# Optimization experiments

Measured on AMD Instinct MI355X. Metric: run time of the kernel, lower is better.

The kernel has to match this reference:

```python
import jax, jax.numpy as jnp
import numpy as np

N_NODES = 100000
N_EDGES = 1600000
IN_CH = 128
OUT_CH = 128
HEADS = 4
HEAD_DIM = OUT_CH // HEADS
NEG_SLOPE_ATT = 0.2   # GATConv default negative_slope
NEG_SLOPE_ACT = 0.2   # block's LeakyReLU(0.2)
BN_EPS = 1e-5


def setup_inputs() -> dict:
    key = jax.random.key(0)
    ks = jax.random.split(key, 6)
    x = jax.random.normal(ks[0], (N_NODES, IN_CH), dtype=jnp.float32)
    edge_index = jax.random.randint(ks[1], (2, N_EDGES), 0, N_NODES, dtype=jnp.int64)
    W = jax.random.normal(ks[2], (IN_CH, HEADS * HEAD_DIM), dtype=jnp.float32) * (1.0 / np.sqrt(IN_CH))
    att_src = jax.random.normal(ks[3], (HEADS, HEAD_DIM), dtype=jnp.float32) * 0.1
    att_dst = jax.random.normal(ks[4], (HEADS, HEAD_DIM), dtype=jnp.float32) * 0.1
    bias = jnp.zeros((OUT_CH,), dtype=jnp.float32)
    gamma = jnp.ones((OUT_CH,), dtype=jnp.float32)
    beta = jnp.zeros((OUT_CH,), dtype=jnp.float32)
    return {"x": x, "edge_index": edge_index, "W": W, "att_src": att_src,
            "att_dst": att_dst, "bias": bias, "gamma": gamma, "beta": beta}


def reference(x, edge_index, W, att_src, att_dst, bias, gamma, beta):
    N = x.shape[0]
    H, C = att_src.shape
    src, dst = edge_index[0], edge_index[1]

    # linear projection per head: [N, H, C]
    h = (x @ W).reshape(N, H, C)

    # per-node attention contributions (alpha_src[i] + alpha_dst[j] on edges)
    a_src = jnp.einsum('nhc,hc->nh', h, att_src)  # [N, H]
    a_dst = jnp.einsum('nhc,hc->nh', h, att_dst)  # [N, H]

    # per-edge raw score, leaky relu (GAT attention nonlinearity)
    e = jax.nn.leaky_relu(a_src[src] + a_dst[dst], NEG_SLOPE_ATT)  # [E, H]

    # segment softmax over edges grouped by destination node
    e_max = jax.ops.segment_max(e, dst, num_segments=N)            # [N, H]
    e_max = jnp.where(jnp.isfinite(e_max), e_max, 0.0)
    ex = jnp.exp(e - e_max[dst])                                   # [E, H]
    denom = jax.ops.segment_sum(ex, dst, num_segments=N)           # [N, H]
    alpha = ex / (denom[dst] + 1e-16)                              # [E, H]

    # scatter-add aggregation of alpha-weighted source features
    msg = alpha[:, :, None] * h[src]                               # [E, H, C]
    out = jax.ops.segment_sum(msg, dst, num_segments=N)            # [N, H, C]
    out = out.reshape(N, H * C) + bias                             # concat heads + bias

    # BatchNorm1d (training mode: batch statistics, biased variance)
    mu = out.mean(axis=0)
    var = out.var(axis=0)
    out = (out - mu) * jax.lax.rsqrt(var + BN_EPS) * gamma + beta

    return jax.nn.leaky_relu(out, NEG_SLOPE_ACT)
```

## Files before the change

### kernel.cpp

```cpp
#include <hip/hip_runtime.h>
#include <hip/hip_fp16.h>
#include <math.h>


#define WAVE  64
#define SHIFT 8
#define CAP   4608
#define CPAD  16
#define FBLK  512

__device__ __forceinline__ float4 leaky4(float4 v, float s) {
    v.x = v.x > 0.f ? v.x : s * v.x;
    v.y = v.y > 0.f ? v.y : s * v.y;
    v.z = v.z > 0.f ? v.z : s * v.z;
    v.w = v.w > 0.f ? v.w : s * v.w;
    return v;
}

__global__ __launch_bounds__(256) void k_gemm_att(
    const float* __restrict__ x, const float* __restrict__ W,
    const float* __restrict__ att_src, const float* __restrict__ att_dst,
    __half* __restrict__ h16, float* __restrict__ a_src, float* __restrict__ a_dst,
    int* __restrict__ cursor, int czero, int N)
{
    __shared__ float xsT[128][36];
    __shared__ float Wl[64][128];

    const int t = threadIdx.x;
    const int row0 = blockIdx.x * 32;

    if (blockIdx.x == 0) {
        for (int i = t; i < czero; i += 256) cursor[i] = 0;
    }

    {
        const int r  = t >> 3;
        const int k0 = (t & 7) * 16;
        const int rr = min(row0 + r, N - 1);
        const float4* xp = (const float4*)(x + (size_t)rr * 128 + k0);
        float4 v0 = xp[0], v1 = xp[1], v2 = xp[2], v3 = xp[3];
        float tmp[16] = {v0.x,v0.y,v0.z,v0.w, v1.x,v1.y,v1.z,v1.w,
                         v2.x,v2.y,v2.z,v2.w, v3.x,v3.y,v3.z,v3.w};
        #pragma unroll
        for (int i = 0; i < 16; ++i) xsT[k0 + i][r] = tmp[i];
    }

    const int tx = t & 31;
    const int ty = t >> 5;
    float acc[4][4] = {{0.f}};

    for (int kt = 0; kt < 2; ++kt) {
        __syncthreads();
        {
            const float4* wp = (const float4*)(W + kt * 64 * 128);
            float4* wl = (float4*)&Wl[0][0];
            #pragma unroll
            for (int i = 0; i < 8; ++i) wl[t + 256 * i] = wp[t + 256 * i];
        }
        __syncthreads();
        #pragma unroll
        for (int k = 0; k < 64; ++k) {
            float4 wv = *(const float4*)&Wl[k][tx * 4];
            float4 xv = *(const float4*)&xsT[kt * 64 + k][ty * 4];
            float xa[4] = {xv.x, xv.y, xv.z, xv.w};
            float wa[4] = {wv.x, wv.y, wv.z, wv.w};
            #pragma unroll
            for (int i = 0; i < 4; ++i)
                #pragma unroll
                for (int j = 0; j < 4; ++j)
                    acc[i][j] = fmaf(xa[i], wa[j], acc[i][j]);
        }
    }

    const int head = tx >> 3;
    const float4 s4 = *(const float4*)&att_src[head * 32 + (tx & 7) * 4];
    const float4 d4 = *(const float4*)&att_dst[head * 32 + (tx & 7) * 4];

    #pragma unroll
    for (int i = 0; i < 4; ++i) {
        const int n = row0 + ty * 4 + i;
        if (n < N) {
            union { __half2 h2[2]; uint2 u; } pk;
            pk.h2[0] = __floats2half2_rn(acc[i][0], acc[i][1]);
            pk.h2[1] = __floats2half2_rn(acc[i][2], acc[i][3]);
            *(uint2*)(h16 + (size_t)n * 128 + tx * 4) = pk.u;
        }
        float ss = acc[i][0]*s4.x + acc[i][1]*s4.y + acc[i][2]*s4.z + acc[i][3]*s4.w;
        float dd = acc[i][0]*d4.x + acc[i][1]*d4.y + acc[i][2]*d4.z + acc[i][3]*d4.w;
        #pragma unroll
        for (int off = 1; off < 8; off <<= 1) {
            ss += __shfl_xor(ss, off);
            dd += __shfl_xor(dd, off);
        }
        if ((tx & 7) == 0 && n < N) {
            a_src[n * 4 + head] = ss;
            a_dst[n * 4 + head] = dd;
        }
    }
}

__global__ __launch_bounds__(256) void k_bucket(
    const int* __restrict__ src, const int* __restrict__ dst,
    int* __restrict__ cursor, int* __restrict__ pairs, int E, int nbkt)
{
    __shared__ int hist[512];
    __shared__ int lcur[512];
    const int t = threadIdx.x;
    hist[t] = 0; hist[t + 256] = 0;
    __syncthreads();

    const int base = blockIdx.x * 2048;
    int sr[8], dr[8];
    #pragma unroll
    for (int i = 0; i < 8; ++i) {
        const int e = base + i * 256 + t;
        if (e < E) { sr[i] = src[e]; dr[i] = dst[e]; }
        else       { sr[i] = -1;     dr[i] = -1; }
    }
    #pragma unroll
    for (int i = 0; i < 8; ++i)
        if (dr[i] >= 0) atomicAdd(&hist[dr[i] >> SHIFT], 1);
    __syncthreads();

    for (int b = t; b < nbkt; b += 256) {
        const int hcount = hist[b];
        lcur[b] = (hcount > 0) ? atomicAdd(&cursor[b * CPAD], hcount) + b * CAP
                               : b * CAP;
    }
    __syncthreads();

    #pragma unroll
    for (int i = 0; i < 8; ++i) {
        if (dr[i] >= 0) {
            const int b = dr[i] >> SHIFT;
            const int pos = atomicAdd(&lcur[b], 1);
            if (pos < b * CAP + CAP)
                pairs[pos] = sr[i] | ((dr[i] & 255) << 20);
        }
    }
}

__global__ __launch_bounds__(FBLK) void k_fine(
    const int* __restrict__ cursor, const int* __restrict__ pairs,
    int* __restrict__ offsets, int* __restrict__ deg,
    int* __restrict__ perm_src, float* __restrict__ bn_sums, int N)
{
    __shared__ int stage[CAP];
    __shared__ int cnt[256];
    __shared__ int scn[256];
    __shared__ int cur[256];

    const int t = threadIdx.x;
    const int b = blockIdx.x;

    if (b == 0 && t < 256) bn_sums[t] = 0.f;

    const int cnt_b = min(cursor[b * CPAD], CAP);
    const int pbase = b * CAP;

    if (t < 256) cnt[t] = 0;
    __syncthreads();

    for (int i = t; i < cnt_b; i += FBLK) {
        const int v = pairs[pbase + i];
        stage[i] = v;
        atomicAdd(&cnt[v >> 20], 1);
    }
    __syncthreads();

    const int v0 = (t < 256) ? cnt[t] : 0;
    if (t < 256) scn[t] = v0;
    __syncthreads();
    for (int off = 1; off < 256; off <<= 1) {
        const int add = (t < 256 && t >= off) ? scn[t - off] : 0;
        __syncthreads();
        if (t < 256) scn[t] += add;
        __syncthreads();
    }
    if (t < 256) {
        const int excl = scn[t] - v0;
        const int node = (b << SHIFT) + t;
        if (node < N) {
            offsets[node] = pbase + excl;
            deg[node]     = v0;
        }
        cur[t] = pbase + excl;
    }
    __syncthreads();

    for (int i = t; i < cnt_b; i += FBLK) {
        const int v = stage[i];
        const int pos = atomicAdd(&cur[v >> 20], 1);
        perm_src[pos] = v & 0xFFFFF;
    }
}

__global__ __launch_bounds__(256) void k_aggregate(
    const int* __restrict__ offsets, const int* __restrict__ deg,
    const int* __restrict__ perm_src,
    const float* __restrict__ a_src, const float* __restrict__ a_dst,
    const __half* __restrict__ h16, float* __restrict__ out, int N)
{
    __shared__ int    ls_s [4][2][32];
    __shared__ float4 ls_ex[4][2][32];

    const int wv   = threadIdx.x >> 6;
    const int lane = threadIdx.x & 63;
    const int nd   = lane >> 5;
    const int l32  = lane & 31;
    const int n    = blockIdx.x * 8 + wv * 2 + nd;
    const bool valid = (n < N);

    const int beg = valid ? offsets[n] : 0;
    const int dg  = valid ? deg[n]     : 0;
    const float4 ad = valid ? *(const float4*)(a_dst + n * 4)
                            : make_float4(0.f, 0.f, 0.f, 0.f);

    const int ph  = (lane >> 4) & 1;
    const int l16 = lane & 15;
    const int ch  = l16 * 8;
    const int hd  = l16 >> 2;
    float acc[8] = {0.f,0.f,0.f,0.f,0.f,0.f,0.f,0.f};
    float dsum = 0.f;

    const int dgmax = max(dg, __shfl_xor(dg, 32));

    for (int base = 0; base < dgmax; base += 32) {
        const int idx = base + l32;
        int s = 0;
        float4 ex = make_float4(0.f, 0.f, 0.f, 0.f);
        if (idx < dg) {
            s = perm_src[beg + idx];
            float4 as = *(const float4*)(a_src + s * 4);
            float4 e = leaky4(make_float4(as.x+ad.x, as.y+ad.y, as.z+ad.z, as.w+ad.w), 0.2f);
            ex.x = __expf(e.x); ex.y = __expf(e.y);
            ex.z = __expf(e.z); ex.w = __expf(e.w);
        }
        ls_s [wv][nd][l32] = s;
        ls_ex[wv][nd][l32] = ex;

        int cn = dg - base;
        cn = (cn < 0) ? 0 : ((cn > 32) ? 32 : cn);
        const int cnmax = max(cn, __shfl_xor(cn, 32));
        const int cnr = (cnmax + 3) & ~3;

        #pragma unroll 2
        for (int t = 0; t < cnr; t += 2) {
            const int slot = t + ph;
            const int   sj  = ls_s[wv][nd][slot];
            const float exj = ((const float*)&ls_ex[wv][nd][slot])[hd];
            union { uint4 u; __half2 h2[4]; } pk;
            pk.u = *(const uint4*)(h16 + (size_t)sj * 128 + ch);
            acc[0] = fmaf(__low2float (pk.h2[0]), exj, acc[0]);
            acc[1] = fmaf(__high2float(pk.h2[0]), exj, acc[1]);
            acc[2] = fmaf(__low2float (pk.h2[1]), exj, acc[2]);
            acc[3] = fmaf(__high2float(pk.h2[1]), exj, acc[3]);
            acc[4] = fmaf(__low2float (pk.h2[2]), exj, acc[4]);
            acc[5] = fmaf(__high2float(pk.h2[2]), exj, acc[5]);
            acc[6] = fmaf(__low2float (pk.h2[3]), exj, acc[6]);
            acc[7] = fmaf(__high2float(pk.h2[3]), exj, acc[7]);
            dsum += exj;
        }
    }

    #pragma unroll
    for (int c = 0; c < 8; ++c) acc[c] += __shfl_xor(acc[c], 16);
    dsum += __shfl_xor(dsum, 16);

    if (ph == 0 && valid) {
        const float inv = 1.0f / (dsum + 1e-16f);
        float* op = out + (size_t)n * 128 + ch;
        *(float4*)(op)     = make_float4(acc[0]*inv, acc[1]*inv, acc[2]*inv, acc[3]*inv);
        *(float4*)(op + 4) = make_float4(acc[4]*inv, acc[5]*inv, acc[6]*inv, acc[7]*inv);
    }
}

__global__ __launch_bounds__(256) void k_bnstats(const float* __restrict__ out,
                                                 float* __restrict__ sums, int N)
{
    const int c    = threadIdx.x & 127;
    const int half = threadIdx.x >> 7;
    float s = 0.f, sq = 0.f;
    for (int r = blockIdx.x * 2 + half; r < N; r += gridDim.x * 2) {
        float v = out[(size_t)r * 128 + c];
        s += v;
        sq = fmaf(v, v, sq);
    }
    __shared__ float ls[256], lq[256];
    ls[threadIdx.x] = s; lq[threadIdx.x] = sq;
    __syncthreads();
    if (half == 0) {
        s  += ls[threadIdx.x + 128];
        sq += lq[threadIdx.x + 128];
        atomicAdd(&sums[c], s);
        atomicAdd(&sums[128 + c], sq);
    }
}

__global__ __launch_bounds__(256) void k_bnapply(float* __restrict__ out,
                                                 const float* __restrict__ sums,
                                                 const float* __restrict__ gamma,
                                                 const float* __restrict__ beta,
                                                 int N)
{
    const int i = blockIdx.x * 256 + threadIdx.x;
    const int total = N * 128;
    if (i >= total) return;
    const int c = i & 127;
    const float invN = 1.0f / (float)N;
    float mu  = sums[c] * invN;
    float var = sums[128 + c] * invN - mu * mu;
    float v = out[i];
    float y = (v - mu) * rsqrtf(var + 1e-5f) * gamma[c] + beta[c];
    out[i] = y > 0.f ? y : 0.2f * y;
}

extern "C" void kernel_launch(void* const* d_in, const int* in_sizes, int n_in,
                              void* d_out, int out_size, void* d_ws, size_t ws_size,
                              hipStream_t stream)
{
    const float* x     = (const float*)d_in[0];
    const int*   ei    = (const int*)  d_in[1];
    const float* W     = (const float*)d_in[2];
    const float* att_s = (const float*)d_in[3];
    const float* att_d = (const float*)d_in[4];
    const float* gamma = (const float*)d_in[6];
    const float* beta  = (const float*)d_in[7];
    float* out = (float*)d_out;

    const int N = in_sizes[0] / 128;
    const int E = in_sizes[1] / 2;
    const int nbkt = (N + (1 << SHIFT) - 1) >> SHIFT;

    char* ws = (char*)d_ws;
    size_t off = 0;
    auto carve = [&](size_t bytes) {
        char* p = ws + off;
        off += (bytes + 255) & ~(size_t)255;
        return p;
    };
    __half* h16      = (__half*)carve((size_t)N * 128 * 2);
    float* a_src     = (float*)carve((size_t)N * 4 * 4);
    float* a_dst     = (float*)carve((size_t)N * 4 * 4);
    int*   offsets   = (int*)  carve((size_t)N * 4);
    int*   deg       = (int*)  carve((size_t)N * 4);
    int*   cursor    = (int*)  carve((size_t)nbkt * CPAD * 4);
    float* bn_sums   = (float*)carve(256 * 4);
    int*   pairs     = (int*)  carve((size_t)nbkt * CAP * 4);
    int*   perm_src  = (int*)  carve((size_t)nbkt * CAP * 4);

    k_gemm_att<<<(N + 31) / 32, 256, 0, stream>>>(x, W, att_s, att_d, h16, a_src, a_dst,
                                                  cursor, nbkt * CPAD, N);
    k_bucket<<<(E + 2047) / 2048, 256, 0, stream>>>(ei, ei + E, cursor, pairs, E, nbkt);
    k_fine<<<nbkt, FBLK, 0, stream>>>(cursor, pairs, offsets, deg, perm_src, bn_sums, N);
    k_aggregate<<<(N + 7) / 8, 256, 0, stream>>>(offsets, deg, perm_src, a_src, a_dst, h16, out, N);
    k_bnstats<<<512, 256, 0, stream>>>(out, bn_sums, N);
    k_bnapply<<<(N * 128 + 255) / 256, 256, 0, stream>>>(out, bn_sums, gamma, beta, N);
}
```

Before: 339.7 us.

## Use split-bf16 MFMA for projection GEMM and move attention dots to separate kernel

Replaces the FP32 FMA tiled GEMM with MFMA bf16 instructions, using a hi/lo split (three MFMAs per tile) to approximate FP32 accuracy. Each block now handles 128 rows, and W is converted to bf16 hi/lo in shared memory once per block. The per-node attention scores are now computed by a new kernel that reads back the fp16 h, rather than in the GEMM epilogue. This adds an extra launch and an extra pass over h, uses the fp16-rounded h for the attention scores, and the h16 stores become scalar 2-byte writes.

```diff
diff --git a/kernel.cpp b/kernel.cpp
--- a/kernel.cpp
+++ b/kernel.cpp
@@ -8,6 +8,9 @@
 #define CAP   4608
 #define CPAD  16
 #define FBLK  512
+
+typedef __attribute__((ext_vector_type(8))) short short8v;
+typedef __attribute__((ext_vector_type(4))) float f32x4;
 
 __device__ __forceinline__ float4 leaky4(float4 v, float s) {
     v.x = v.x > 0.f ? v.x : s * v.x;
@@ -17,85 +20,134 @@
     return v;
 }
 
-__global__ __launch_bounds__(256) void k_gemm_att(
+__device__ __forceinline__ unsigned short f2bf(float f) {
+    unsigned int u = __float_as_uint(f);
+    u += 0x7FFFu + ((u >> 16) & 1u);
+    return (unsigned short)(u >> 16);
+}
+__device__ __forceinline__ float bf2f(unsigned short h) {
+    return __uint_as_float(((unsigned int)h) << 16);
+}
+__device__ __forceinline__ void cvt8(float4 a, float4 b, short8v& hi, short8v& lo) {
+    float f[8] = {a.x, a.y, a.z, a.w, b.x, b.y, b.z, b.w};
+    #pragma unroll
+    for (int j = 0; j < 8; ++j) {
+        unsigned short h = f2bf(f[j]);
+        hi[j] = (short)h;
+        lo[j] = (short)f2bf(f[j] - bf2f(h));
+    }
+}
+
+__global__ __launch_bounds__(256) void k_gemm(
     const float* __restrict__ x, const float* __restrict__ W,
-    const float* __restrict__ att_src, const float* __restrict__ att_dst,
-    __half* __restrict__ h16, float* __restrict__ a_src, float* __restrict__ a_dst,
-    int* __restrict__ cursor, int czero, int N)
-{
-    __shared__ float xsT[128][36];
-    __shared__ float Wl[64][128];
+    __half* __restrict__ h16, int* __restrict__ cursor, int czero, int N)
+{
+    __shared__ short8v WB[2][32][64];
 
     const int t = threadIdx.x;
-    const int row0 = blockIdx.x * 32;
-
     if (blockIdx.x == 0) {
         for (int i = t; i < czero; i += 256) cursor[i] = 0;
     }
 
     {
-        const int r  = t >> 3;
-        const int k0 = (t & 7) * 16;
-        const int rr = min(row0 + r, N - 1);
-        const float4* xp = (const float4*)(x + (size_t)rr * 128 + k0);
-        float4 v0 = xp[0], v1 = xp[1], v2 = xp[2], v3 = xp[3];
-        float tmp[16] = {v0.x,v0.y,v0.z,v0.w, v1.x,v1.y,v1.z,v1.w,
-                         v2.x,v2.y,v2.z,v2.w, v3.x,v3.y,v3.z,v3.w};
+        const int lane = t & 63;
+        const int w    = t >> 6;
         #pragma unroll
-        for (int i = 0; i < 16; ++i) xsT[k0 + i][r] = tmp[i];
-    }
-
-    const int tx = t & 31;
-    const int ty = t >> 5;
-    float acc[4][4] = {{0.f}};
-
-    for (int kt = 0; kt < 2; ++kt) {
-        __syncthreads();
-        {
-            const float4* wp = (const float4*)(W + kt * 64 * 128);
-            float4* wl = (float4*)&Wl[0][0];
+        for (int rep = 0; rep < 8; ++rep) {
+            const int region = rep * 4 + w;
+            const int kt = region >> 3, n = region & 7;
+            const int krow = kt * 32 + ((lane >> 4) << 3);
+            const int col  = n * 16 + (lane & 15);
+            short8v hi, lo;
             #pragma unroll
-            for (int i = 0; i < 8; ++i) wl[t + 256 * i] = wp[t + 256 * i];
-        }
-        __syncthreads();
+            for (int j = 0; j < 8; ++j) {
+                const float wv = W[(krow + j) * 128 + col];
+                const unsigned short hb = f2bf(wv);
+                hi[j] = (short)hb;
+                lo[j] = (short)f2bf(wv - bf2f(hb));
+            }
+            WB[0][region][lane] = hi;
+            WB[1][region][lane] = lo;
+        }
+    }
+    __syncthreads();
+
+    const int lane = t & 63;
+    const int wv_  = t >> 6;
+    const int jcol = lane & 15;
+    const int rg   = lane >> 4;
+    const int rowbase = blockIdx.x * 128 + wv_ * 32;
+
+    const int arow0 = min(rowbase + jcol,      N - 1);
+    const int arow1 = min(rowbase + 16 + jcol, N - 1);
+
+    f32x4 acc0[8] = {};
+    f32x4 acc1[8] = {};
+
+    #pragma unroll
+    for (int kt = 0; kt < 4; ++kt) {
+        const int k0 = kt * 32 + rg * 8;
+        const float* xp0 = x + (size_t)arow0 * 128 + k0;
+        const float* xp1 = x + (size_t)arow1 * 128 + k0;
+        short8v ah0, al0, ah1, al1;
+        cvt8(*(const float4*)xp0, *(const float4*)(xp0 + 4), ah0, al0);
+        cvt8(*(const float4*)xp1, *(const float4*)(xp1 + 4), ah1, al1);
         #pragma unroll
-        for (int k = 0; k < 64; ++k) {
-            float4 wv = *(const float4*)&Wl[k][tx * 4];
-            float4 xv = *(const float4*)&xsT[kt * 64 + k][ty * 4];
-            float xa[4] = {xv.x, xv.y, xv.z, xv.w};
-            float wa[4] = {wv.x, wv.y, wv.z, wv.w};
-            #pragma unroll
-            for (int i = 0; i < 4; ++i)
-                #pragma unroll
-                for (int j = 0; j < 4; ++j)
-                    acc[i][j] = fmaf(xa[i], wa[j], acc[i][j]);
-        }
-    }
-
-    const int head = tx >> 3;
-    const float4 s4 = *(const float4*)&att_src[head * 32 + (tx & 7) * 4];
-    const float4 d4 = *(const float4*)&att_dst[head * 32 + (tx & 7) * 4];
-
-    #pragma unroll
-    for (int i = 0; i < 4; ++i) {
-        const int n = row0 + ty * 4 + i;
-        if (n < N) {
-            union { __half2 h2[2]; uint2 u; } pk;
-            pk.h2[0] = __floats2half2_rn(acc[i][0], acc[i][1]);
-            pk.h2[1] = __floats2half2_rn(acc[i][2], acc[i][3]);
-            *(uint2*)(h16 + (size_t)n * 128 + tx * 4) = pk.u;
-        }
-        float ss = acc[i][0]*s4.x + acc[i][1]*s4.y + acc[i][2]*s4.z + acc[i][3]*s4.w;
-        float dd = acc[i][0]*d4.x + acc[i][1]*d4.y + acc[i][2]*d4.z + acc[i][3]*d4.w;
+        for (int n = 0; n < 8; ++n) {
+            const short8v bh = WB[0][kt * 8 + n][lane];
+            const short8v bl = WB[1][kt * 8 + n][lane];
+            acc0[n] = __builtin_amdgcn_mfma_f32_16x16x32_bf16(ah0, bh, acc0[n], 0, 0, 0);
+            acc0[n] = __builtin_amdgcn_mfma_f32_16x16x32_bf16(ah0, bl, acc0[n], 0, 0, 0);
+            acc0[n] = __builtin_amdgcn_mfma_f32_16x16x32_bf16(al0, bh, acc0[n], 0, 0, 0);
+            acc1[n] = __builtin_amdgcn_mfma_f32_16x16x32_bf16(ah1, bh, acc1[n], 0, 0, 0);
+            acc1[n] = __builtin_amdgcn_mfma_f32_16x16x32_bf16(ah1, bl, acc1[n], 0, 0, 0);
+            acc1[n] = __builtin_amdgcn_mfma_f32_16x16x32_bf16(al1, bh, acc1[n], 0, 0, 0);
+        }
+    }
+
+    #pragma unroll
+    for (int r = 0; r < 4; ++r) {
+        const int row0 = rowbase + rg * 4 + r;
+        const int row1 = row0 + 16;
         #pragma unroll
-        for (int off = 1; off < 8; off <<= 1) {
-            ss += __shfl_xor(ss, off);
-            dd += __shfl_xor(dd, off);
-        }
-        if ((tx & 7) == 0 && n < N) {
-            a_src[n * 4 + head] = ss;
-            a_dst[n * 4 + head] = dd;
-        }
+        for (int n = 0; n < 8; ++n) {
+            if (row0 < N) h16[(size_t)row0 * 128 + n * 16 + jcol] = __float2half(acc0[n][r]);
+            if (row1 < N) h16[(size_t)row1 * 128 + n * 16 + jcol] = __float2half(acc1[n][r]);
+        }
+    }
+}
+
+__global__ __launch_bounds__(256) void k_att(
+    const __half* __restrict__ h16,
+    const float* __restrict__ att_src, const float* __restrict__ att_dst,
+    float* __restrict__ a_src, float* __restrict__ a_dst, int N)
+{
+    const int t    = threadIdx.x;
+    const int node = blockIdx.x * 32 + (t >> 3);
+    const int t8   = t & 7;
+    if (node >= N) return;
+    const int head = t8 >> 1;
+
+    union { uint4 u[2]; __half2 h2[8]; } pk;
+    const uint4* hp = (const uint4*)(h16 + (size_t)node * 128 + t8 * 16);
+    pk.u[0] = hp[0];
+    pk.u[1] = hp[1];
+
+    const float* asp = att_src + head * 32 + (t8 & 1) * 16;
+    const float* adp = att_dst + head * 32 + (t8 & 1) * 16;
+
+    float ps = 0.f, pd = 0.f;
+    #pragma unroll
+    for (int i = 0; i < 8; ++i) {
+        const float2 hv = __half22float2(pk.h2[i]);
+        ps += hv.x * asp[i * 2] + hv.y * asp[i * 2 + 1];
+        pd += hv.x * adp[i * 2] + hv.y * adp[i * 2 + 1];
+    }
+    ps += __shfl_xor(ps, 1);
+    pd += __shfl_xor(pd, 1);
+    if ((t8 & 1) == 0) {
+        a_src[node * 4 + head] = ps;
+        a_dst[node * 4 + head] = pd;
     }
 }
 
@@ -349,8 +401,8 @@
     int*   pairs     = (int*)  carve((size_t)nbkt * CAP * 4);
     int*   perm_src  = (int*)  carve((size_t)nbkt * CAP * 4);
 
-    k_gemm_att<<<(N + 31) / 32, 256, 0, stream>>>(x, W, att_s, att_d, h16, a_src, a_dst,
-                                                  cursor, nbkt * CPAD, N);
+    k_gemm<<<(N + 127) / 128, 256, 0, stream>>>(x, W, h16, cursor, nbkt * CPAD, N);
+    k_att<<<(N + 31) / 32, 256, 0, stream>>>(h16, att_s, att_d, a_src, a_dst, N);
     k_bucket<<<(E + 2047) / 2048, 256, 0, stream>>>(ei, ei + E, cursor, pairs, E, nbkt);
     k_fine<<<nbkt, FBLK, 0, stream>>>(cursor, pairs, offsets, deg, perm_src, bn_sums, N);
     k_aggregate<<<(N + 7) / 8, 256, 0, stream>>>(offsets, deg, perm_src, a_src, a_dst, h16, out, N);
```

Measured after the change: 318.0 us. -6.4%, faster.
